# Kernel tuning notes

Measured on AMD Instinct MI355X. Metric: run time of the kernel, lower is better.

Reference implementation:

```python
import jax, jax.numpy as jnp
import numpy as np

V, N, D, H, C = 3, 4096, 512, 128, 5  # views, nodes, in_dim, hidden, classes
NEG = -9.0e15   # mask value from original code (-9000000000000000.0)
NEG_SLOPE = 0.25


def _leaky(x, slope):
    return jnp.where(x >= 0, x, slope * x)


def setup_inputs() -> dict:
    key = jax.random.key(0)
    ks = jax.random.split(key, 24)
    g = lambda i, shape, s=0.05: (jax.random.normal(ks[i], shape, dtype=jnp.float32) * s)
    return {
        "data": jax.random.normal(ks[0], (V, N, D), dtype=jnp.float32),
        "adj": jax.random.randint(ks[1], (V, N, N), 0, 2, dtype=jnp.int32),
        "gac_w": g(2, (V, D, H)), "gac_b": g(3, (V, H)),
        "a1": g(4, (V, H)), "a2": g(5, (V, H)),
        "mlp_w": g(6, (V, D, H)), "mlp_b": g(7, (V, H)),
        "q_w": g(8, (V, H, H)), "q_b": g(9, (V, H)),
        "k_w": g(10, (V, H, H)), "k_b": g(11, (V, H)),
        "v_w": g(12, (V, H, H)), "v_b": g(13, (V, H)),
        "fc_w": g(14, (V, H, H)), "fc_b": g(15, (V, H)),
        "conf_w": g(16, (V, H, 1)), "conf_b": g(17, (V, 1)),
        "mm_w": g(18, (V * H, C)), "mm_b": g(19, (C,)),
    }


def reference(data, adj, gac_w, gac_b, a1, a2, mlp_w, mlp_b,
              q_w, q_b, k_w, k_b, v_w, v_b, fc_w, fc_b,
              conf_w, conf_b, mm_w, mm_b):
    # --- GraphAttentionConv (per view, vectorized over v) ---
    h = jnp.einsum('vnd,vdh->vnh', data, gac_w)               # spmm(input, W)
    e1 = jnp.einsum('vnh,vh->vn', h, a1)                      # h @ a1
    e2 = jnp.einsum('vnh,vh->vn', h, a2)                      # h @ a2
    e = _leaky(e1[:, :, None] + e2[:, None, :], NEG_SLOPE)    # [V,N,N] broadcast-add
    e = jnp.where(adj > 0, e, NEG)                            # mask by dense adjacency
    att = jax.nn.softmax(e, axis=-1)                          # row softmax
    feat = jnp.einsum('vnm,vmh->vnh', att, h) + gac_b[:, None, :]
    feat = _leaky(feat, NEG_SLOPE)                            # F.leaky_relu(GAC out, 0.25)
    # residual MLP branch
    feat = feat + jnp.einsum('vnd,vdh->vnh', data, mlp_w) + mlp_b[:, None, :]

    # --- StructureGuidedFeatureEnhancement (n_heads=1): per-node HxH attention ---
    Q = jnp.einsum('vnh,vho->vno', feat, q_w) + q_b[:, None, :]
    K = jnp.einsum('vnh,vho->vno', feat, k_w) + k_b[:, None, :]
    Vv = jnp.einsum('vnh,vho->vno', feat, v_w) + v_b[:, None, :]
    scale = jnp.sqrt(jnp.asarray(H, jnp.float32))
    A = Q[:, :, :, None] * K[:, :, None, :] / scale           # [V,N,H,H] outer product
    A = jax.nn.softmax(A, axis=-1)
    agg = jnp.einsum('vnio,vno->vni', A, Vv)                  # attention @ V
    agg = jnp.einsum('vnh,vho->vno', agg, fc_w) + fc_b[:, None, :]
    feat = jax.nn.relu(agg)

    # --- TCP confidence gating ---
    conf = jnp.einsum('vnh,vho->vno', feat, conf_w) + conf_b[:, None, :]  # [V,N,1]
    feat = feat * conf

    # --- concat views along feature dim, final classifier ---
    mm = jnp.transpose(feat, (1, 0, 2)).reshape(N, V * H)     # [N, V*H]
    return mm @ mm_w + mm_b                                   # MMlogit [N, C]
```

## Files before the change

### kernel.cpp

```cpp
#include <hip/hip_runtime.h>
#include <hip/hip_bf16.h>

#define V 3
#define N 4096
#define D 512
#define H 128
#define C 5
#define KS 2
#define M2 64
#define M1 32
#define LOG2E 1.4426950408889634f

typedef short short8 __attribute__((ext_vector_type(8)));
typedef float floatx4 __attribute__((ext_vector_type(4)));
typedef int   intx4  __attribute__((ext_vector_type(4)));

__device__ __forceinline__ unsigned short f2bf(float f){
  __hip_bfloat16 h = __float2bfloat16(f);
  return *reinterpret_cast<unsigned short*>(&h);
}
__device__ __forceinline__ unsigned int pk_bf16(float a, float b){
  unsigned int ua = __float_as_uint(a), ub = __float_as_uint(b);
  ua += 0x7FFFu + ((ua >> 16) & 1u);
  ub += 0x7FFFu + ((ub >> 16) & 1u);
  return (ua >> 16) | (ub & 0xFFFF0000u);
}

__global__ __launch_bounds__(256) void k0_all(
    const float* __restrict__ gw, const float* __restrict__ mw,
    const float* __restrict__ qw, const float* __restrict__ kw,
    const float* __restrict__ vw, const float* __restrict__ fw,
    unsigned short* __restrict__ wT, unsigned short* __restrict__ wq4T)
{
  const int b = blockIdx.x, t = threadIdx.x;
  __shared__ unsigned short tr[128*72];
  const float* src;
  unsigned short* dst0;
  int K, koff;
  if (b < 48){
    const int v = b % V, r = b / V, m = r & 1, kc = r >> 1;
    src  = (m ? mw : gw) + (size_t)v*D*H + (size_t)kc*64*H;
    dst0 = wT + ((size_t)m*V + v)*(size_t)H*D;
    K = D; koff = kc*64;
  } else {
    const int j = b - 48, v = j % V, r = j / V, m = r & 3, kc = r >> 2;
    src  = (m==0?qw: m==1?kw: m==2?vw: fw) + (size_t)v*H*H + (size_t)kc*64*H;
    dst0 = wq4T + ((size_t)m*V + v)*(size_t)H*H;
    K = H; koff = kc*64;
  }
  for (int i = t; i < 64*128; i += 256){
    int kk = i >> 7, col = i & 127;
    tr[col*72 + kk] = f2bf(src[i]);
  }
  __syncthreads();
  const int col = t >> 1, half = t & 1;
  uint4* dst = (uint4*)(dst0 + (size_t)col*K + koff + half*32);
  const unsigned short* s = &tr[col*72 + half*32];
  dst[0] = *(const uint4*)(s);
  dst[1] = *(const uint4*)(s + 8);
  dst[2] = *(const uint4*)(s + 16);
  dst[3] = *(const uint4*)(s + 24);
}

__global__ __launch_bounds__(512) void k1_gemm(
    const float* __restrict__ data, const unsigned short* __restrict__ wT,
    const float* __restrict__ a1, const float* __restrict__ a2,
    unsigned short* __restrict__ hT, float* __restrict__ mlp_out,
    float* __restrict__ e1g, float* __restrict__ e2g)
{
  const int v = blockIdx.y;
  const int n0 = blockIdx.x * M1;
  const int t = threadIdx.x;
  const int w = t >> 6, l = t & 63;
  __shared__ __align__(16) unsigned short AT[2][16][64][8];
  __shared__ float epart[2][M1][4];
  unsigned short* hTile = &AT[0][0][0][0];

  {
    const int r = t >> 4, oct = t & 15;
    const float4* dp = (const float4*)(data + ((size_t)v*N + n0 + r)*D + oct*32);
    float4 f[8];
    #pragma unroll
    for (int i=0;i<8;i++) f[i] = dp[i];
    #pragma unroll
    for (int q=0;q<4;q++){
      uint4 u;
      u.x = pk_bf16(f[2*q].x,   f[2*q].y);
      u.y = pk_bf16(f[2*q].z,   f[2*q].w);
      u.z = pk_bf16(f[2*q+1].x, f[2*q+1].y);
      u.w = pk_bf16(f[2*q+1].z, f[2*q+1].w);
      *(uint4*)&AT[r>>4][oct][(r&15) + 16*q][0] = u;
    }
  }
  __syncthreads();
  const int m = w >> 2, cb = (w & 3)*32;
  const int quad = l >> 4, c16 = l & 15;
  const unsigned short* b0 = wT + (((size_t)m*V + v)*H + cb + c16)*D + quad*8;
  floatx4 acc[2][2];
  #pragma unroll
  for (int rt=0;rt<2;rt++) for (int c=0;c<2;c++) acc[rt][c] = (floatx4){0.f,0.f,0.f,0.f};
  #pragma unroll
  for (int ks=0; ks<16; ks++){
    short8 a0 = *(const short8*)&AT[0][ks][l][0];
    short8 a1f = *(const short8*)&AT[1][ks][l][0];
    short8 bb0 = *(const short8*)(b0 + ks*32);
    short8 bb1 = *(const short8*)(b0 + 16*D + ks*32);
    acc[0][0] = __builtin_amdgcn_mfma_f32_16x16x32_bf16(a0,  bb0, acc[0][0], 0,0,0);
    acc[1][0] = __builtin_amdgcn_mfma_f32_16x16x32_bf16(a1f, bb0, acc[1][0], 0,0,0);
    acc[0][1] = __builtin_amdgcn_mfma_f32_16x16x32_bf16(a0,  bb1, acc[0][1], 0,0,0);
    acc[1][1] = __builtin_amdgcn_mfma_f32_16x16x32_bf16(a1f, bb1, acc[1][1], 0,0,0);
  }
  if (m == 1){
    #pragma unroll
    for (int rt=0;rt<2;rt++)
      #pragma unroll
      for (int c=0;c<2;c++)
        #pragma unroll
        for (int reg=0;reg<4;reg++){
          const int row = rt*16 + quad*4 + reg, col = cb + c*16 + c16;
          mlp_out[((size_t)v*N + n0 + row)*H + col] = acc[rt][c][reg];
        }
  } else {
    const float a1v0 = a1[v*H + cb + c16],      a2v0 = a2[v*H + cb + c16];
    const float a1v1 = a1[v*H + cb + 16 + c16], a2v1 = a2[v*H + cb + 16 + c16];
    #pragma unroll
    for (int rt=0;rt<2;rt++)
      #pragma unroll
      for (int reg=0;reg<4;reg++){
        float p1 = acc[rt][0][reg]*a1v0 + acc[rt][1][reg]*a1v1;
        float p2 = acc[rt][0][reg]*a2v0 + acc[rt][1][reg]*a2v1;
        p1 += __shfl_xor(p1,1); p1 += __shfl_xor(p1,2);
        p1 += __shfl_xor(p1,4); p1 += __shfl_xor(p1,8);
        p2 += __shfl_xor(p2,1); p2 += __shfl_xor(p2,2);
        p2 += __shfl_xor(p2,4); p2 += __shfl_xor(p2,8);
        if (c16 == 0){
          epart[0][rt*16 + quad*4 + reg][w] = p1;
          epart[1][rt*16 + quad*4 + reg][w] = p2;
        }
      }
  }
  __syncthreads();
  if (m == 0){
    #pragma unroll
    for (int rt=0;rt<2;rt++)
      #pragma unroll
      for (int c=0;c<2;c++)
        #pragma unroll
        for (int reg=0;reg<4;reg++){
          const int row = rt*16 + quad*4 + reg, col = cb + c*16 + c16;
          hTile[col*40 + row] = f2bf(acc[rt][c][reg]);
        }
  }
  __syncthreads();
  if (t < 128){
    const unsigned short* s = &hTile[t*40];
    uint4* dst = (uint4*)(hT + ((size_t)v*H + t)*N + n0);
    dst[0] = *(const uint4*)(s);
    dst[1] = *(const uint4*)(s + 8);
    dst[2] = *(const uint4*)(s + 16);
    dst[3] = *(const uint4*)(s + 24);
  } else if (t < 128 + M1){
    const int r = t - 128;
    e1g[(size_t)v*N + n0 + r] = LOG2E*(epart[0][r][0]+epart[0][r][1]+epart[0][r][2]+epart[0][r][3]);
  } else if (t < 128 + 2*M1){
    const int r = t - 128 - M1;
    e2g[(size_t)v*N + n0 + r] = LOG2E*(epart[1][r][0]+epart[1][r][1]+epart[1][r][2]+epart[1][r][3]);
  }
}

__global__ __launch_bounds__(512, 4) void k2_attn(
    const unsigned short* __restrict__ hT, const int* __restrict__ adj,
    const float* __restrict__ e1g, const float* __restrict__ e2g,
    float* __restrict__ pacc, float* __restrict__ pdenG)
{
  const int v = blockIdx.z;
  const int ksid = blockIdx.y;
  const int n0 = blockIdx.x * M2;
  const int kbase = ksid * (N/KS);
  const int t = threadIdx.x;
  const int w = t >> 6, l = t & 63;
  __shared__ __align__(16) unsigned short Afrag[2][4][4][64][8];
  __shared__ float pden_sh[M2][4];

  const int ksl  = w & 3;
  const int quad = l >> 4;
  const int rt0  = w >> 2;
  const int row0 = rt0*16 + (l & 15);
  const int row1 = row0 + 32;
  const int koff = ksl*32 + quad*8;
  const intx4* ap0 = (const intx4*)(adj + ((size_t)v*N + n0 + row0)*N + kbase + koff);
  const intx4* ap1 = (const intx4*)(adj + ((size_t)v*N + n0 + row1)*N + kbase + koff);
  const float4* ep = (const float4*)(e2g + (size_t)v*N + kbase + koff);
  const float e1r0 = e1g[(size_t)v*N + n0 + row0];
  const float e1r1 = e1g[(size_t)v*N + n0 + row1];
  float psum0 = 0.f, psum1 = 0.f;

  const int col = w*16 + (l & 15);
  const unsigned short* bcol = hT + ((size_t)v*H + col)*N + kbase + quad*8;
  floatx4 acc[4];
  #pragma unroll
  for (int rt=0;rt<4;rt++) acc[rt] = (floatx4){0.f,0.f,0.f,0.f};

  intx4  a00 = __builtin_nontemporal_load(ap0);
  intx4  a01 = __builtin_nontemporal_load(ap0 + 1);
  intx4  a10 = __builtin_nontemporal_load(ap1);
  intx4  a11 = __builtin_nontemporal_load(ap1 + 1);
  float4 ev0 = ep[0];
  float4 ev1 = ep[1];

  const int NCH = (N/KS)/128;
  #pragma unroll 1
  for (int c = 0; c < NCH; c++){
    const int buf = c & 1;
    {
      float ev[8] = {ev0.x,ev0.y,ev0.z,ev0.w, ev1.x,ev1.y,ev1.z,ev1.w};
      int   aa[8] = {a00.x,a00.y,a00.z,a00.w, a01.x,a01.y,a01.z,a01.w};
      int   bb[8] = {a10.x,a10.y,a10.z,a10.w, a11.x,a11.y,a11.z,a11.w};
      float wa[8], wb[8];
      #pragma unroll
      for (int j=0;j<8;j++){
        float ya = e1r0 + ev[j];
        ya = fmaxf(ya, 0.25f*ya);
        float ea = exp2f(ya);
        wa[j] = (aa[j] > 0) ? ea : 0.f;
        psum0 += wa[j];
        float yb = e1r1 + ev[j];
        yb = fmaxf(yb, 0.25f*yb);
        float eb = exp2f(yb);
        wb[j] = (bb[j] > 0) ? eb : 0.f;
        psum1 += wb[j];
      }
      union { short8 s; unsigned int u[4]; } pa, pb;
      #pragma unroll
      for (int j=0;j<4;j++){
        pa.u[j] = pk_bf16(wa[2*j], wa[2*j+1]);
        pb.u[j] = pk_bf16(wb[2*j], wb[2*j+1]);
      }
      *(short8*)&Afrag[buf][rt0  ][ksl][l][0] = pa.s;
      *(short8*)&Afrag[buf][rt0+2][ksl][l][0] = pb.s;
    }
    if (c+1 < NCH){
      a00 = __builtin_nontemporal_load(ap0 + (c+1)*32);
      a01 = __builtin_nontemporal_load(ap0 + (c+1)*32 + 1);
      a10 = __builtin_nontemporal_load(ap1 + (c+1)*32);
      a11 = __builtin_nontemporal_load(ap1 + (c+1)*32 + 1);
      ev0 = ep[(c+1)*32];
      ev1 = ep[(c+1)*32 + 1];
    }
    __syncthreads();
    #pragma unroll
    for (int ks=0; ks<4; ks++){
      short8 b8 = *(const short8*)(bcol + c*128 + ks*32);
      #pragma unroll
      for (int rt=0; rt<4; rt++){
        short8 a8 = *(const short8*)&Afrag[buf][rt][ks][l][0];
        acc[rt] = __builtin_amdgcn_mfma_f32_16x16x32_bf16(a8, b8, acc[rt], 0, 0, 0);
      }
    }
    __syncthreads();
  }
  psum0 += __shfl_xor(psum0, 16);
  psum0 += __shfl_xor(psum0, 32);
  psum1 += __shfl_xor(psum1, 16);
  psum1 += __shfl_xor(psum1, 32);
  if (l < 16){
    pden_sh[row0][ksl] = psum0;
    pden_sh[row1][ksl] = psum1;
  }
  __syncthreads();
  const size_t pb = ((size_t)v*KS + ksid)*(N/M2) + blockIdx.x;
  float* pa = pacc + pb*(M2*H);
  #pragma unroll
  for (int rt=0; rt<4; rt++){
    #pragma unroll
    for (int reg=0; reg<4; reg++){
      const int row = rt*16 + quad*4 + reg;
      pa[row*H + col] = acc[rt][reg];
    }
  }
  if (t < M2){
    float den = pden_sh[t][0] + pden_sh[t][1] + pden_sh[t][2] + pden_sh[t][3];
    pdenG[pb*M2 + t] = den;
  }
}

__global__ __launch_bounds__(256) void k3_sgfe(
    const float* __restrict__ pacc, const float* __restrict__ pdenG,
    const float* __restrict__ mlp_out,
    const float* __restrict__ gac_b, const float* __restrict__ mlp_b,
    const unsigned short* __restrict__ wq4T,
    const float* __restrict__ qb, const float* __restrict__ kb,
    const float* __restrict__ vb, const float* __restrict__ fcb,
    const float* __restrict__ confw, const float* __restrict__ confb,
    float* __restrict__ feat2)
{
  const int v = blockIdx.y;
  const int n0 = blockIdx.x * 16;
  const int t = threadIdx.x;
  const int w = t >> 6, l = t & 63;
  const int c16 = l & 15, quad = l >> 4;
  __shared__ __align__(16) unsigned short Ffrag[4][64][8];
  __shared__ __align__(16) unsigned short Gfrag[4][64][8];
  __shared__ float Qs[16][H];
  __shared__ float2 KVs[16][H];
  __shared__ float pc[16][4];
  __shared__ float confs[16];

  {
    const int col = t & 127, rh = t >> 7;
    const int bx2 = blockIdx.x >> 2;
    const int lr0 = (blockIdx.x & 3) * 16;
    const float gbv = gac_b[v*H + col];
    const float mbv = mlp_b[v*H + col];
    const int ks = col >> 5, q2 = (col & 31) >> 3, j = col & 7;
    #pragma unroll
    for (int i=0;i<8;i++){
      const int r = rh*8 + i;
      float num = 0.f, den = 0.f;
      #pragma unroll
      for (int s=0;s<KS;s++){
        const size_t pb = ((size_t)v*KS + s)*(N/M2) + bx2;
        num += pacc[pb*(M2*H) + (size_t)(lr0+r)*H + col];
        den += pdenG[pb*M2 + lr0 + r];
      }
      float x = num/den + gbv;
      x = (x >= 0.f) ? x : 0.25f*x;
      x += mlp_out[((size_t)v*N + n0 + r)*H + col] + mbv;
      Ffrag[ks][r + 16*q2][j] = f2bf(x);
    }
  }
  __syncthreads();
  const int colw0 = 2*w*16 + c16;
  const float QSC = 0.08838834764831845f * LOG2E;
  {
    const unsigned short* bq = wq4T + (((size_t)0*V + v)*H + colw0)*H + quad*8;
    const unsigned short* bk = wq4T + (((size_t)1*V + v)*H + colw0)*H + quad*8;
    const unsigned short* bv = wq4T + (((size_t)2*V + v)*H + colw0)*H + quad*8;
    floatx4 aq[2], ak[2], av[2];
    #pragma unroll
    for (int c=0;c<2;c++){ aq[c]=(floatx4){0,0,0,0}; ak[c]=(floatx4){0,0,0,0}; av[c]=(floatx4){0,0,0,0}; }
    #pragma unroll
    for (int ks=0; ks<4; ks++){
      short8 a8 = *(const short8*)&Ffrag[ks][l][0];
      #pragma unroll
      for (int c=0;c<2;c++){
        short8 q8 = *(const short8*)(bq + (size_t)c*16*H + ks*32);
        short8 k8 = *(const short8*)(bk + (size_t)c*16*H + ks*32);
        short8 v8 = *(const short8*)(bv + (size_t)c*16*H + ks*32);
        aq[c] = __builtin_amdgcn_mfma_f32_16x16x32_bf16(a8, q8, aq[c], 0,0,0);
        ak[c] = __builtin_amdgcn_mfma_f32_16x16x32_bf16(a8, k8, ak[c], 0,0,0);
        av[c] = __builtin_amdgcn_mfma_f32_16x16x32_bf16(a8, v8, av[c], 0,0,0);
      }
    }
    #pragma unroll
    for (int c=0;c<2;c++){
      const int col = colw0 + c*16;
      const float qbv = qb[v*H+col], kbv = kb[v*H+col], vbv = vb[v*H+col];
      #pragma unroll
      for (int reg=0;reg<4;reg++){
        const int node = quad*4 + reg;
        Qs[node][col] = (aq[c][reg] + qbv) * QSC;
        KVs[node][col] = make_float2(ak[c][reg] + kbv, av[c][reg] + vbv);
      }
    }
  }
  __syncthreads();
  #pragma unroll
  for (int p=0;p<4;p++){
    const int r = 4*w + p;
    const float qa  = Qs[r][l];
    const float qb2 = Qs[r][l+64];
    float sA=0.f, aA=0.f, sB=0.f, aB=0.f;
    const float4* kvp = (const float4*)&KVs[r][0];
    #pragma unroll 4
    for (int oo=0; oo<H/2; oo++){
      float4 kv2 = kvp[oo];
      float eA0 = exp2f(qa*kv2.x);  sA += eA0; aA = fmaf(eA0, kv2.y, aA);
      float eA1 = exp2f(qa*kv2.z);  sA += eA1; aA = fmaf(eA1, kv2.w, aA);
      float eB0 = exp2f(qb2*kv2.x); sB += eB0; aB = fmaf(eB0, kv2.y, aB);
      float eB1 = exp2f(qb2*kv2.z); sB += eB1; aB = fmaf(eB1, kv2.w, aB);
    }
    Gfrag[l>>5][r + 16*((l&31)>>3)][l&7] = f2bf(aA/sA);
    Gfrag[2 + (l>>5)][r + 16*((l&31)>>3)][l&7] = f2bf(aB/sB);
  }
  __syncthreads();
  const unsigned short* bf = wq4T + (((size_t)3*V + v)*H + colw0)*H + quad*8;
  floatx4 af[2];
  af[0]=(floatx4){0,0,0,0}; af[1]=(floatx4){0,0,0,0};
  #pragma unroll
  for (int ks=0; ks<4; ks++){
    short8 a8 = *(const short8*)&Gfrag[ks][l][0];
    #pragma unroll
    for (int c=0;c<2;c++){
      short8 b8 = *(const short8*)(bf + (size_t)c*16*H + ks*32);
      af[c] = __builtin_amdgcn_mfma_f32_16x16x32_bf16(a8, b8, af[c], 0,0,0);
    }
  }
  float g[2][4];
  float pn[4] = {0.f,0.f,0.f,0.f};
  #pragma unroll
  for (int c=0;c<2;c++){
    const int col = colw0 + c*16;
    const float fcbv = fcb[v*H+col];
    const float cwv  = confw[v*H+col];
    #pragma unroll
    for (int reg=0;reg<4;reg++){
      float gg = fmaxf(af[c][reg] + fcbv, 0.f);
      g[c][reg] = gg;
      pn[reg] += gg*cwv;
    }
  }
  #pragma unroll
  for (int reg=0;reg<4;reg++){
    pn[reg] += __shfl_xor(pn[reg], 1);
    pn[reg] += __shfl_xor(pn[reg], 2);
    pn[reg] += __shfl_xor(pn[reg], 4);
    pn[reg] += __shfl_xor(pn[reg], 8);
  }
  if (c16 == 0){
    #pragma unroll
    for (int reg=0;reg<4;reg++) pc[quad*4 + reg][w] = pn[reg];
  }
  __syncthreads();
  if (t < 16) confs[t] = pc[t][0] + pc[t][1] + pc[t][2] + pc[t][3] + confb[v];
  __syncthreads();
  #pragma unroll
  for (int c=0;c<2;c++){
    const int col = colw0 + c*16;
    #pragma unroll
    for (int reg=0;reg<4;reg++){
      const int node = quad*4 + reg;
      feat2[((size_t)v*N + n0 + node)*H + col] = g[c][reg]*confs[node];
    }
  }
}

__global__ __launch_bounds__(256) void k4_cls(
    const float* __restrict__ feat2,
    const float* __restrict__ mm_w, const float* __restrict__ mm_b,
    float* __restrict__ out)
{
  const int n = blockIdx.x*4 + (threadIdx.x >> 6);
  const int t = threadIdx.x & 63;
  float a[C] = {0,0,0,0,0};
  for (int j=t; j<V*H; j+=64){
    int vv = j >> 7, hh = j & (H-1);
    float f = feat2[((size_t)vv*N + n)*H + hh];
    #pragma unroll
    for (int c=0;c<C;c++) a[c] = fmaf(f, mm_w[j*C+c], a[c]);
  }
  #pragma unroll
  for (int c=0;c<C;c++){
    #pragma unroll
    for (int o=32;o>0;o>>=1) a[c] += __shfl_down(a[c],o);
  }
  if (t==0){
    #pragma unroll
    for (int c=0;c<C;c++) out[(size_t)n*C+c] = a[c] + mm_b[c];
  }
}

extern "C" void kernel_launch(void* const* d_in, const int* in_sizes, int n_in,
                              void* d_out, int out_size, void* d_ws, size_t ws_size,
                              hipStream_t stream)
{
  (void)in_sizes; (void)n_in; (void)out_size; (void)ws_size;
  const float* data  = (const float*)d_in[0];
  const int*   adj   = (const int*)d_in[1];
  const float* gac_w = (const float*)d_in[2];
  const float* gac_b = (const float*)d_in[3];
  const float* a1    = (const float*)d_in[4];
  const float* a2    = (const float*)d_in[5];
  const float* mlp_w = (const float*)d_in[6];
  const float* mlp_b = (const float*)d_in[7];
  const float* q_w   = (const float*)d_in[8];
  const float* q_b   = (const float*)d_in[9];
  const float* k_w   = (const float*)d_in[10];
  const float* k_b   = (const float*)d_in[11];
  const float* v_w   = (const float*)d_in[12];
  const float* v_b   = (const float*)d_in[13];
  const float* fc_w  = (const float*)d_in[14];
  const float* fc_b  = (const float*)d_in[15];
  const float* cw    = (const float*)d_in[16];
  const float* cb    = (const float*)d_in[17];
  const float* mm_w  = (const float*)d_in[18];
  const float* mm_b  = (const float*)d_in[19];

  float* ws = (float*)d_ws;
  const size_t VNH = (size_t)V*N*H;
  float* mlp   = ws;
  float* feat2 = ws + VNH;
  float* e1    = ws + 2*VNH;
  float* e2    = e1 + (size_t)V*N;
  unsigned short* hT   = (unsigned short*)(e2 + (size_t)V*N);
  unsigned short* wT   = hT + VNH;
  unsigned short* wq4T = wT + (size_t)2*V*H*D;
  float* pacc  = (float*)(wq4T + (size_t)4*V*H*H);
  float* pden  = pacc + (size_t)V*KS*(N/M2)*M2*H;

  k0_all <<<dim3(72),          256, 0, stream>>>(gac_w, mlp_w, q_w, k_w, v_w, fc_w, wT, wq4T);
  k1_gemm<<<dim3(N/M1, V),     512, 0, stream>>>(data, wT, a1, a2, hT, mlp, e1, e2);
  k2_attn<<<dim3(N/M2, KS, V), 512, 0, stream>>>(hT, adj, e1, e2, pacc, pden);
  k3_sgfe<<<dim3(N/16, V),     256, 0, stream>>>(pacc, pden, mlp, gac_b, mlp_b,
                                                 wq4T, q_b, k_b, v_b, fc_b,
                                                 cw, cb, feat2);
  k4_cls <<<dim3(N/4),         256, 0, stream>>>(feat2, mm_w, mm_b, (float*)d_out);
}
```

Baseline: 440.9 us.

## Fuse classifier into SGFE kernel with atomics and raise attention K-split

The final classifier kernel is removed. Each SGFE block now multiplies its gated features by the matching slice of mm_w and atomically adds per-node class partials into the output, which the attention kernel pre-initialises with the bias. This drops the feat2 round trip through global memory and one launch. The attention K-split also goes from 2 to 4, giving more blocks at the cost of more partial accumulators for k3 to reduce. Float atomics make the summation order nondeterministic, and k3 must correctly merge 4 splits, which the hidden code presumably handles through KS.

```diff
diff --git a/kernel.cpp b/kernel.cpp
--- a/kernel.cpp
+++ b/kernel.cpp
@@ -6,7 +6,7 @@
 #define D 512
 #define H 128
 #define C 5
-#define KS 2
+#define KS 4
 #define M2 64
 #define M1 32
 #define LOG2E 1.4426950408889634f
@@ -171,7 +171,8 @@
 __global__ __launch_bounds__(512, 4) void k2_attn(
     const unsigned short* __restrict__ hT, const int* __restrict__ adj,
     const float* __restrict__ e1g, const float* __restrict__ e2g,
-    float* __restrict__ pacc, float* __restrict__ pdenG)
+    float* __restrict__ pacc, float* __restrict__ pdenG,
+    const float* __restrict__ mm_b, float* __restrict__ outg)
 {
   const int v = blockIdx.z;
   const int ksid = blockIdx.y;
@@ -282,6 +283,10 @@
     float den = pden_sh[t][0] + pden_sh[t][1] + pden_sh[t][2] + pden_sh[t][3];
     pdenG[pb*M2 + t] = den;
   }
+  if (blockIdx.y == 0 && blockIdx.z == 0){
+    const int idx = blockIdx.x * 512 + t;
+    if (idx < N*C) outg[idx] = mm_b[idx % C];
+  }
 }
 
 __global__ __launch_bounds__(256) void k3_sgfe(
@@ -292,7 +297,7 @@
     const float* __restrict__ qb, const float* __restrict__ kb,
     const float* __restrict__ vb, const float* __restrict__ fcb,
     const float* __restrict__ confw, const float* __restrict__ confb,
-    float* __restrict__ feat2)
+    const float* __restrict__ mm_w, float* __restrict__ outg)
 {
   const int v = blockIdx.y;
   const int n0 = blockIdx.x * 16;
@@ -424,40 +429,32 @@
   __syncthreads();
   if (t < 16) confs[t] = pc[t][0] + pc[t][1] + pc[t][2] + pc[t][3] + confb[v];
   __syncthreads();
+  float pcls[4][C];
+  #pragma unroll
+  for (int reg=0;reg<4;reg++)
+    #pragma unroll
+    for (int cc=0;cc<C;cc++) pcls[reg][cc] = 0.f;
   #pragma unroll
   for (int c=0;c<2;c++){
     const int col = colw0 + c*16;
+    const float* mwp = mm_w + (size_t)(v*H + col)*C;
     #pragma unroll
     for (int reg=0;reg<4;reg++){
-      const int node = quad*4 + reg;
-      feat2[((size_t)v*N + n0 + node)*H + col] = g[c][reg]*confs[node];
-    }
-  }
-}
-
-__global__ __launch_bounds__(256) void k4_cls(
-    const float* __restrict__ feat2,
-    const float* __restrict__ mm_w, const float* __restrict__ mm_b,
-    float* __restrict__ out)
-{
-  const int n = blockIdx.x*4 + (threadIdx.x >> 6);
-  const int t = threadIdx.x & 63;
-  float a[C] = {0,0,0,0,0};
-  for (int j=t; j<V*H; j+=64){
-    int vv = j >> 7, hh = j & (H-1);
-    float f = feat2[((size_t)vv*N + n)*H + hh];
-    #pragma unroll
-    for (int c=0;c<C;c++) a[c] = fmaf(f, mm_w[j*C+c], a[c]);
-  }
-  #pragma unroll
-  for (int c=0;c<C;c++){
-    #pragma unroll
-    for (int o=32;o>0;o>>=1) a[c] += __shfl_down(a[c],o);
-  }
-  if (t==0){
-    #pragma unroll
-    for (int c=0;c<C;c++) out[(size_t)n*C+c] = a[c] + mm_b[c];
-  }
+      const float val = g[c][reg]*confs[quad*4 + reg];
+      #pragma unroll
+      for (int cc=0;cc<C;cc++) pcls[reg][cc] = fmaf(val, mwp[cc], pcls[reg][cc]);
+    }
+  }
+  #pragma unroll
+  for (int reg=0;reg<4;reg++)
+    #pragma unroll
+    for (int cc=0;cc<C;cc++){
+      float x = pcls[reg][cc];
+      x += __shfl_xor(x,1); x += __shfl_xor(x,2);
+      x += __shfl_xor(x,4); x += __shfl_xor(x,8);
+      if (c16 == 0)
+        atomicAdd(&outg[(size_t)(n0 + quad*4 + reg)*C + cc], x);
+    }
 }
 
 extern "C" void kernel_launch(void* const* d_in, const int* in_sizes, int n_in,
@@ -489,8 +486,7 @@
   float* ws = (float*)d_ws;
   const size_t VNH = (size_t)V*N*H;
   float* mlp   = ws;
-  float* feat2 = ws + VNH;
-  float* e1    = ws + 2*VNH;
+  float* e1    = ws + VNH;
   float* e2    = e1 + (size_t)V*N;
   unsigned short* hT   = (unsigned short*)(e2 + (size_t)V*N);
   unsigned short* wT   = hT + VNH;
@@ -500,9 +496,9 @@
 
   k0_all <<<dim3(72),          256, 0, stream>>>(gac_w, mlp_w, q_w, k_w, v_w, fc_w, wT, wq4T);
   k1_gemm<<<dim3(N/M1, V),     512, 0, stream>>>(data, wT, a1, a2, hT, mlp, e1, e2);
-  k2_attn<<<dim3(N/M2, KS, V), 512, 0, stream>>>(hT, adj, e1, e2, pacc, pden);
+  k2_attn<<<dim3(N/M2, KS, V), 512, 0, stream>>>(hT, adj, e1, e2, pacc, pden,
+                                                 mm_b, (float*)d_out);
   k3_sgfe<<<dim3(N/16, V),     256, 0, stream>>>(pacc, pden, mlp, gac_b, mlp_b,
                                                  wq4T, q_b, k_b, v_b, fc_b,
-                                                 cw, cb, feat2);
-  k4_cls <<<dim3(N/4),         256, 0, stream>>>(feat2, mm_w, mm_b, (float*)d_out);
-}
+                                                 cw, cb, mm_w, (float*)d_out);
+}
```

Result: no change. 437.1 us (-0.9%).
